# Kernel tuning notes

Measured on AMD Instinct MI355X. Metric: run time of the kernel, lower is better.

The kernel has to match this reference:

```python
import jax, jax.numpy as jnp
import numpy as np

E = 65536      # number of edge tokens
N = 16384      # number of nodes
M = 262144     # number of edge-edge pairs (line-graph edges)
D = 256        # model dim
H = 8          # heads
HD = D // H    # head dim = 32
HID = 4 * D    # ffn hidden = 1024
EPS = 1e-5


def layer_norm(x, scale, bias):
    m = jnp.mean(x, axis=-1, keepdims=True)
    v = jnp.mean(jnp.square(x - m), axis=-1, keepdims=True)
    return (x - m) * jax.lax.rsqrt(v + EPS) * scale + bias


def setup_inputs() -> dict:
    key = jax.random.key(0)
    ks = jax.random.split(key, 24)
    s = 0.02
    inp = {
        'edge_attr': jax.random.normal(ks[0], (E, D), jnp.float32),
        'x': jax.random.normal(ks[1], (N, D), jnp.float32),
        'src_e': jax.random.randint(ks[2], (M,), 0, E),
        'dst_e': jax.random.randint(ks[3], (M,), 0, E),
        'edge_index': jax.random.randint(ks[4], (2, E), 0, N),
        'edge_edge_bias': jax.random.normal(ks[5], (M, H), jnp.float32),
        'ln1_s': jnp.ones((D,), jnp.float32),
        'ln1_b': jnp.zeros((D,), jnp.float32),
        'Wq': jax.random.normal(ks[6], (D, D), jnp.float32) * s,
        'bq': jnp.zeros((D,), jnp.float32),
        'Wk': jax.random.normal(ks[7], (D, D), jnp.float32) * s,
        'bk': jnp.zeros((D,), jnp.float32),
        'Wv': jax.random.normal(ks[8], (D, D), jnp.float32) * s,
        'bv': jnp.zeros((D,), jnp.float32),
        'Wo': jax.random.normal(ks[9], (D, D), jnp.float32) * s,
        'bo': jnp.zeros((D,), jnp.float32),
        'ln2_s': jnp.ones((D,), jnp.float32),
        'ln2_b': jnp.zeros((D,), jnp.float32),
        'W1': jax.random.normal(ks[10], (D, HID), jnp.float32) * s,
        'b1': jnp.zeros((HID,), jnp.float32),
        'W2': jax.random.normal(ks[11], (HID, D), jnp.float32) * s,
        'b2': jnp.zeros((D,), jnp.float32),
        'deg_coef': jax.random.normal(ks[12], (1, D, 2), jnp.float32) * s,
        'We2n': jax.random.normal(ks[13], (D, D), jnp.float32) * s,
        'be2n': jnp.zeros((D,), jnp.float32),
    }
    return inp


def reference(edge_attr, x, src_e, dst_e, edge_index, edge_edge_bias,
              ln1_s, ln1_b, Wq, bq, Wk, bk, Wv, bv, Wo, bo,
              ln2_s, ln2_b, W1, b1, W2, b2, deg_coef, We2n, be2n):
    scale = HD ** (-0.5)
    edge_in = edge_attr  # proj_in is Identity (in_dim == out_dim)

    # --- edge multi-head attention over edge-edge index (pre-LN) ---
    en = layer_norm(edge_in, ln1_s, ln1_b)
    q = (en @ Wq + bq).reshape(E, H, HD)
    k = (en @ Wk + bk).reshape(E, H, HD)
    v = (en @ Wv + bv).reshape(E, H, HD)
    q_dst = q[dst_e]                       # (M, H, HD)
    k_src = k[src_e]
    logits = jnp.sum(q_dst * k_src, axis=-1) * scale + edge_edge_bias  # (M, H)
    # sparse softmax grouped by dst_e (segment softmax with num_segments=E)
    seg_max = jax.ops.segment_max(logits, dst_e, num_segments=E)       # (E, H)
    ex = jnp.exp(logits - seg_max[dst_e])
    seg_sum = jax.ops.segment_sum(ex, dst_e, num_segments=E)
    attn = ex / (seg_sum[dst_e] + 1e-16)                               # (M, H)
    msg = v[src_e] * attn[:, :, None]                                  # (M, H, HD)
    agg = jax.ops.segment_sum(msg, dst_e, num_segments=E).reshape(E, D)
    edge_attn = agg @ Wo + bo
    h1 = edge_in + edge_attn

    # --- FFN (pre-LN), exact GELU as in torch nn.GELU ---
    h1n = layer_norm(h1, ln2_s, ln2_b)
    ffn = jax.nn.gelu(h1n @ W1 + b1, approximate=False) @ W2 + b2
    edge_out = h1 + ffn

    # --- degree scaler: [h, h*log1p(deg_e)] . deg_coef ---
    deg_e = jax.ops.segment_sum(jnp.ones((M,), edge_out.dtype), dst_e, num_segments=E)
    log_deg_e = jnp.log1p(deg_e)[:, None]                              # (E, 1)
    edge_out = edge_out * deg_coef[0, :, 0] + (edge_out * log_deg_e) * deg_coef[0, :, 1]

    # --- edge -> node update (LN output on nodes is unused in the original) ---
    node_msg = (jax.ops.segment_sum(edge_out, edge_index[0], num_segments=N)
                + jax.ops.segment_sum(edge_out, edge_index[1], num_segments=N))
    node_out = x + node_msg @ We2n + be2n

    return edge_out, node_out
```

## Files before the change

### kernel.cpp

```cpp
#include <hip/hip_runtime.h>
#include <math.h>

#define E_ 65536
#define N_ 16384
#define M_ 262144

typedef unsigned short u16;
typedef __attribute__((ext_vector_type(4))) float f32x4;
typedef __attribute__((ext_vector_type(8))) short bf16x8;
typedef __attribute__((ext_vector_type(4))) unsigned short u16x4;
typedef __attribute__((ext_vector_type(2))) unsigned int u32x2;
typedef __attribute__((ext_vector_type(4))) float f4v;

__device__ __forceinline__ float b2f(u16 u) {
    union { unsigned u; float f; } x; x.u = ((unsigned)u) << 16; return x.f;
}
__device__ __forceinline__ u16 f2b(float f) {
    union { float f; unsigned u; } x; x.f = f;
    unsigned r = x.u + 0x7FFFu + ((x.u >> 16) & 1u);
    return (u16)(r >> 16);
}
__device__ __forceinline__ float gelu_f(float x) {
    float y = 1.5957691216057308f * x * (1.0f + 0.044715f * x * x);
    return x * __builtin_amdgcn_rcpf(1.0f + __expf(-y));
}

#define GLDS(gp, lp) __builtin_amdgcn_global_load_lds( \
    (const __attribute__((address_space(1))) void*)(gp), \
    (__attribute__((address_space(3))) void*)(lp), 16, 0, 0)

__global__ void ge_zero(int* __restrict__ p, int n) {
    int i = blockIdx.x * 256 + threadIdx.x;
    if (i < n) p[i] = 0;
}

__global__ void ge_convw(const float* __restrict__ Wq, const float* __restrict__ Wk,
                         const float* __restrict__ Wv, const float* __restrict__ bq,
                         const float* __restrict__ bk, const float* __restrict__ bv,
                         const float* __restrict__ Wo, const float* __restrict__ W1,
                         const float* __restrict__ W2, const float* __restrict__ We2n,
                         u16* __restrict__ WqkvT, float* __restrict__ bqkv,
                         u16* __restrict__ WoT, u16* __restrict__ W1T,
                         u16* __restrict__ W2T, u16* __restrict__ We2nT) {
    long i = (long)blockIdx.x * 256 + threadIdx.x;
    if (i < 196608) {
        int n = (int)(i >> 8), k = (int)(i & 255);
        const float* W = (n < 256) ? Wq : ((n < 512) ? Wk : Wv);
        int nn = n & 255;
        WqkvT[i] = f2b(W[k * 256 + nn]);
        return;
    }
    i -= 196608;
    if (i < 768) { bqkv[i] = (i < 256) ? bq[i] : ((i < 512) ? bk[i - 256] : bv[i - 512]); return; }
    i -= 768;
    if (i < 65536) { int n = (int)(i >> 8), k = (int)(i & 255); WoT[i] = f2b(Wo[k * 256 + n]); return; }
    i -= 65536;
    if (i < 262144) { int n = (int)(i >> 8), k = (int)(i & 255); W1T[i] = f2b(W1[k * 1024 + n]); return; }
    i -= 262144;
    if (i < 262144) {
        int n = (int)(i / 1024), k = (int)(i % 1024);
        int k64 = k & 63, base = k - k64;
        int old_k = base + (k64 & 3) * 16 + (k64 >> 2);
        W2T[i] = f2b(W2[old_k * 256 + n]);
        return;
    }
    i -= 262144;
    if (i < 65536) { int n = (int)(i >> 8), k = (int)(i & 255); We2nT[i] = f2b(We2n[k * 256 + n]); return; }
}

template <int BF16IN>
__global__ __launch_bounds__(256) void ge_ln(const void* __restrict__ in,
                                             const float* __restrict__ s,
                                             const float* __restrict__ b,
                                             u16* __restrict__ out) {
    int tid = threadIdx.x, l = tid & 63, w = tid >> 6;
    long r = (long)blockIdx.x * 4 + w;
    float x0, x1, x2, x3;
    if constexpr (BF16IN) {
        u16x4 xv = *(const u16x4*)&((const u16*)in)[r * 256 + 4 * l];
        x0 = b2f(xv[0]); x1 = b2f(xv[1]); x2 = b2f(xv[2]); x3 = b2f(xv[3]);
    } else {
        f4v x = *(const f4v*)&((const float*)in)[r * 256 + 4 * l];
        x0 = x[0]; x1 = x[1]; x2 = x[2]; x3 = x[3];
    }
    float sum = x0 + x1 + x2 + x3;
#pragma unroll
    for (int off = 1; off < 64; off <<= 1) sum += __shfl_xor(sum, off);
    float mean = sum * (1.0f / 256.0f);
    float d0 = x0 - mean, d1 = x1 - mean, d2 = x2 - mean, d3 = x3 - mean;
    float ss = d0 * d0 + d1 * d1 + d2 * d2 + d3 * d3;
#pragma unroll
    for (int off = 1; off < 64; off <<= 1) ss += __shfl_xor(ss, off);
    float rs = rsqrtf(ss * (1.0f / 256.0f) + 1e-5f);
    u16x4 o;
    o[0] = f2b(d0 * rs * s[4 * l + 0] + b[4 * l + 0]);
    o[1] = f2b(d1 * rs * s[4 * l + 1] + b[4 * l + 1]);
    o[2] = f2b(d2 * rs * s[4 * l + 2] + b[4 * l + 2]);
    o[3] = f2b(d3 * rs * s[4 * l + 3] + b[4 * l + 3]);
    *(u16x4*)&out[r * 256 + 4 * l] = o;
}

__global__ void ge_count(const int* __restrict__ idx, int* __restrict__ cnt, int n) {
    int i = blockIdx.x * 256 + threadIdx.x;
    if (i < n) atomicAdd(&cnt[idx[i]], 1);
}

__global__ __launch_bounds__(256) void ge_bsum(const int* __restrict__ cnt,
                                               int* __restrict__ bsum, int n) {
    int i = blockIdx.x * 256 + threadIdx.x;
    int v = (i < n) ? cnt[i] : 0;
#pragma unroll
    for (int off = 1; off < 64; off <<= 1) v += __shfl_xor(v, off);
    __shared__ int ws_[4];
    int l = threadIdx.x & 63, w = threadIdx.x >> 6;
    if (l == 0) ws_[w] = v;
    __syncthreads();
    if (threadIdx.x == 0) bsum[blockIdx.x] = ws_[0] + ws_[1] + ws_[2] + ws_[3];
}

__global__ __launch_bounds__(256) void ge_bscan(int* __restrict__ bsum, int nb) {
    __shared__ int lds[256];
    int tid = threadIdx.x;
    int v = (tid < nb) ? bsum[tid] : 0;
    lds[tid] = v;
    __syncthreads();
#pragma unroll
    for (int off = 1; off < 256; off <<= 1) {
        int t = (tid >= off) ? lds[tid - off] : 0;
        __syncthreads();
        lds[tid] += t;
        __syncthreads();
    }
    if (tid < nb) bsum[tid] = lds[tid] - v;
}

__global__ __launch_bounds__(256) void ge_cscan(const int* __restrict__ cnt,
                                                const int* __restrict__ bsum,
                                                int* __restrict__ rowStart,
                                                int* __restrict__ cursor,
                                                float* __restrict__ ldeg, int n) {
    __shared__ int lds[256];
    int tid = threadIdx.x;
    int i = blockIdx.x * 256 + tid;
    int c = (i < n) ? cnt[i] : 0;
    lds[tid] = c;
    __syncthreads();
#pragma unroll
    for (int off = 1; off < 256; off <<= 1) {
        int t = (tid >= off) ? lds[tid - off] : 0;
        __syncthreads();
        lds[tid] += t;
        __syncthreads();
    }
    if (i < n) {
        int ex = bsum[blockIdx.x] + lds[tid] - c;
        rowStart[i] = ex;
        cursor[i] = ex;
        if (ldeg) ldeg[i] = log1pf((float)c);
        if (i == n - 1) rowStart[n] = ex + c;
    }
}

__global__ void ge_fill(const int* __restrict__ idx, int* __restrict__ cursor,
                        int* __restrict__ csr, int n, int modE) {
    int i = blockIdx.x * 256 + threadIdx.x;
    if (i < n) {
        int slot = atomicAdd(&cursor[idx[i]], 1);
        csr[slot] = (modE && i >= modE) ? (i - modE) : i;
    }
}

__global__ void ge_fill_attn(const int* __restrict__ dst, const int* __restrict__ src,
                             const float* __restrict__ eeb, int* __restrict__ cursor,
                             int* __restrict__ csrSrc, float* __restrict__ biasCsr, int n) {
    int i = blockIdx.x * 256 + threadIdx.x;
    if (i < n) {
        int slot = atomicAdd(&cursor[dst[i]], 1);
        csrSrc[slot] = src[i];
        f4v b0 = *(const f4v*)&eeb[(size_t)i * 8];
        f4v b1 = *(const f4v*)&eeb[(size_t)i * 8 + 4];
        *(f4v*)&biasCsr[(size_t)slot * 8] = b0;
        *(f4v*)&biasCsr[(size_t)slot * 8 + 4] = b1;
    }
}

template <int EPI>
__global__ __launch_bounds__(256) void ge_gemm(
    const u16* __restrict__ A, const u16* __restrict__ Bt, int K, int nxt,
    const float* __restrict__ bias, const float* __restrict__ res,
    const u16* __restrict__ resB, const float* __restrict__ ldeg,
    const float* __restrict__ dcoef,
    float* __restrict__ outF, u16* __restrict__ outB, u16* __restrict__ outB2,
    int ldOut) {
    __shared__ __align__(16) char smem[32768];
    const int tid = threadIdx.x;
    const int l = tid & 63, w = tid >> 6;
    const int ny = gridDim.x / nxt;
    const int gsz = 64 * ny;
    const int bid = blockIdx.x;
    const int xt = (bid / gsz) * 64 + (bid % gsz) % 64;
    const int yt = (bid % gsz) / 64;
    const int rowBase = xt * 128, colBase = yt * 128;
    const int ar = tid >> 2, aq = tid & 3;
    const int aqs = aq ^ (ar & 3);
    const u16* Ag = A + (size_t)(rowBase + ar) * K + aqs * 8;
    const u16* Bg = Bt + (size_t)(colBase + ar) * K + aqs * 8;
    const size_t row64 = (size_t)64 * K;

    f32x4 acc[4][4] = {};
    const int lr = l & 15;
    const int ks2 = (((l >> 4) ^ (l & 3)) << 3);
    const int wr = (w >> 1) * 64, wc = (w & 1) * 64;
    const int nt = K >> 5;

    auto STAGE = [&](int b, int t) {
        const int kk = t * 32;
        char* dA = smem + b * 8192 + w * 1024;
        char* dB = smem + 16384 + b * 8192 + w * 1024;
        GLDS(Ag + kk, dA);
        GLDS(Ag + kk + row64, dA + 4096);
        GLDS(Bg + kk, dB);
        GLDS(Bg + kk + row64, dB + 4096);
    };

    STAGE(0, 0);
    __syncthreads();
    int cur = 0;
    for (int t = 0; t < nt; ++t) {
        if (t + 1 < nt) STAGE(cur ^ 1, t + 1);
        const u16* bufA = (const u16*)(smem + cur * 8192);
        const u16* bufB = (const u16*)(smem + 16384 + cur * 8192);
        bf16x8 af[4], bfr[4];
#pragma unroll
        for (int mi = 0; mi < 4; mi++) af[mi] = *(const bf16x8*)&bufA[(wr + mi * 16 + lr) * 32 + ks2];
#pragma unroll
        for (int ni = 0; ni < 4; ni++) bfr[ni] = *(const bf16x8*)&bufB[(wc + ni * 16 + lr) * 32 + ks2];
#pragma unroll
        for (int mi = 0; mi < 4; mi++)
#pragma unroll
            for (int ni = 0; ni < 4; ni++)
                acc[mi][ni] = __builtin_amdgcn_mfma_f32_16x16x32_bf16(af[mi], bfr[ni], acc[mi][ni], 0, 0, 0);
        if (t + 1 < nt) {
            __syncthreads();
            cur ^= 1;
        }
    }

    const int r0 = (l >> 4) * 4;
    if constexpr (EPI == 2) {
        float bv[4];
#pragma unroll
        for (int ni = 0; ni < 4; ni++) bv[ni] = bias[colBase + wc + ni * 16 + lr];
#pragma unroll
        for (int mi = 0; mi < 4; mi++) {
#pragma unroll
            for (int r = 0; r < 4; r++) {
                int grow = rowBase + wr + mi * 16 + r0 + r;
                float v0 = gelu_f(acc[mi][0][r] + bv[0]);
                float v1 = gelu_f(acc[mi][1][r] + bv[1]);
                float v2 = gelu_f(acc[mi][2][r] + bv[2]);
                float v3 = gelu_f(acc[mi][3][r] + bv[3]);
                unsigned lo, hi;
                asm("v_cvt_pk_bf16_f32 %0, %1, %2" : "=v"(lo) : "v"(v0), "v"(v1));
                asm("v_cvt_pk_bf16_f32 %0, %1, %2" : "=v"(hi) : "v"(v2), "v"(v3));
                u32x2 pk; pk[0] = lo; pk[1] = hi;
                *(u32x2*)&outB[(size_t)grow * 1024 + colBase + wc + lr * 4] = pk;
            }
        }
    } else if constexpr (EPI == 5) {
        __syncthreads();
        u16* ep = (u16*)smem;
#pragma unroll
        for (int mi = 0; mi < 4; mi++) {
#pragma unroll
            for (int ni = 0; ni < 4; ni++) {
#pragma unroll
                for (int r = 0; r < 4; r++) {
                    int rl = wr + mi * 16 + r0 + r;
                    int cl = wc + ni * 16 + lr;
                    float c = acc[mi][ni][r] + bias[colBase + cl];
                    ep[rl * 128 + (cl ^ (((rl >> 2) & 3) << 4))] = f2b(c);
                }
            }
        }
        __syncthreads();
#pragma unroll
        for (int j = 0; j < 8; j++) {
            int lin = tid + j * 256;
            int row = lin >> 4, ch = lin & 15;
            int grow = rowBase + row;
            bf16x8 v = *(const bf16x8*)&ep[row * 128 + ((ch * 8) ^ (((row >> 2) & 3) << 4))];
            int gcol0 = colBase + ch * 8;
            u16x4 vlo = *((const u16x4*)&v);
            u16x4 vhi = *(((const u16x4*)&v) + 1);
            if (gcol0 < 256) {
                *(bf16x8*)&outB[(size_t)grow * 256 + gcol0] = v;
            } else if (gcol0 < 512) {
                int d0 = (gcol0 - 256) >> 2;
                *(u16x4*)&outB2[(size_t)grow * 512 + 8 * d0] = vlo;
                *(u16x4*)&outB2[(size_t)grow * 512 + 8 * (d0 + 1)] = vhi;
            } else {
                int d0 = (gcol0 - 512) >> 2;
                *(u16x4*)&outB2[(size_t)grow * 512 + 8 * d0 + 4] = vlo;
                *(u16x4*)&outB2[(size_t)grow * 512 + 8 * (d0 + 1) + 4] = vhi;
            }
        }
    } else {
#pragma unroll
        for (int mi = 0; mi < 4; mi++) {
#pragma unroll
            for (int ni = 0; ni < 4; ni++) {
#pragma unroll
                for (int r = 0; r < 4; r++) {
                    int grow = rowBase + wr + mi * 16 + r0 + r;
                    int gcol = colBase + wc + ni * 16 + lr;
                    float c = acc[mi][ni][r];
                    if constexpr (EPI == 1) {
                        outB[(size_t)grow * ldOut + gcol] =
                            f2b(c + bias[gcol] + res[(size_t)grow * 256 + gcol]);
                    } else if constexpr (EPI == 3) {
                        float t2 = c + bias[gcol] + b2f(resB[(size_t)grow * 256 + gcol]);
                        outF[(size_t)grow * ldOut + gcol] =
                            t2 * (dcoef[2 * gcol] + ldeg[grow] * dcoef[2 * gcol + 1]);
                    } else {
                        outF[(size_t)grow * ldOut + gcol] =
                            c + bias[gcol] + res[(size_t)grow * 256 + gcol];
                    }
                }
            }
        }
    }
}

__global__ __launch_bounds__(256) void ge_attn(const u16* __restrict__ qb,
                                               const u16* __restrict__ kvb,
                                               const float* __restrict__ biasCsr,
                                               const int* __restrict__ csrSrc,
                                               const int* __restrict__ rowStart,
                                               u16* __restrict__ agg) {
    int tid = threadIdx.x, l = tid & 63, w = tid >> 6;
    int e = blockIdx.x * 4 + w;
    int g = l >> 3;
    const float scale = 0.17677669529663687f;
    u16x4 qv = *(const u16x4*)&qb[(size_t)e * 256 + 4 * l];
    float q0 = b2f(qv[0]), q1 = b2f(qv[1]), q2 = b2f(qv[2]), q3 = b2f(qv[3]);
    int s0 = rowStart[e], s1 = rowStart[e + 1];

    float sum = 0.0f, a0 = 0.0f, a1 = 0.0f, a2 = 0.0f, a3 = 0.0f;
    if (s0 < s1) {
        int sc = csrSrc[s0];
        bf16x8 kvc = *(const bf16x8*)&kvb[(size_t)sc * 512 + 8 * l];
        float bc = biasCsr[(size_t)s0 * 8 + g];
        for (int i = s0; i < s1; i++) {
            int inx = (i + 1 < s1) ? (i + 1) : i;
            int sn = csrSrc[inx];
            bf16x8 kvn = *(const bf16x8*)&kvb[(size_t)sn * 512 + 8 * l];
            float bn = biasCsr[(size_t)inx * 8 + g];
            float p = q0 * b2f((u16)kvc[0]) + q1 * b2f((u16)kvc[1]) +
                      q2 * b2f((u16)kvc[2]) + q3 * b2f((u16)kvc[3]);
            p += __shfl_xor(p, 1);
            p += __shfl_xor(p, 2);
            p += __shfl_xor(p, 4);
            float ex = __expf(p * scale + bc);
            sum += ex;
            a0 += ex * b2f((u16)kvc[4]);
            a1 += ex * b2f((u16)kvc[5]);
            a2 += ex * b2f((u16)kvc[6]);
            a3 += ex * b2f((u16)kvc[7]);
            kvc = kvn;
            bc = bn;
        }
    }
    float inv = 1.0f / (sum + 1e-16f);
    u16x4 o;
    o[0] = f2b(a0 * inv);
    o[1] = f2b(a1 * inv);
    o[2] = f2b(a2 * inv);
    o[3] = f2b(a3 * inv);
    *(u16x4*)&agg[(size_t)e * 256 + 4 * l] = o;
}

__global__ __launch_bounds__(256) void ge_nodeagg(const float* __restrict__ edge_out,
                                                  const int* __restrict__ rowStart,
                                                  const int* __restrict__ csr,
                                                  u16* __restrict__ nmsg) {
    int tid = threadIdx.x, l = tid & 63, w = tid >> 6;
    int n = blockIdx.x * 4 + w;
    int s0 = rowStart[n], s1 = rowStart[n + 1];
    float a0 = 0.0f, a1 = 0.0f, a2 = 0.0f, a3 = 0.0f;
    for (int i = s0; i < s1; i++) {
        int e = csr[i];
        f4v v = *(const f4v*)&edge_out[(size_t)e * 256 + 4 * l];
        a0 += v[0]; a1 += v[1]; a2 += v[2]; a3 += v[3];
    }
    u16x4 o;
    o[0] = f2b(a0); o[1] = f2b(a1); o[2] = f2b(a2); o[3] = f2b(a3);
    *(u16x4*)&nmsg[(size_t)n * 256 + 4 * l] = o;
}

extern "C" void kernel_launch(void* const* d_in, const int* in_sizes, int n_in,
                              void* d_out, int out_size, void* d_ws, size_t ws_size,
                              hipStream_t stream) {
    (void)in_sizes; (void)n_in; (void)out_size; (void)ws_size;
    const float* edge_attr = (const float*)d_in[0];
    const float* x = (const float*)d_in[1];
    const int* src_e = (const int*)d_in[2];
    const int* dst_e = (const int*)d_in[3];
    const int* edge_index = (const int*)d_in[4];
    const float* eeb = (const float*)d_in[5];
    const float* ln1_s = (const float*)d_in[6];
    const float* ln1_b = (const float*)d_in[7];
    const float* Wq = (const float*)d_in[8];
    const float* bq = (const float*)d_in[9];
    const float* Wk = (const float*)d_in[10];
    const float* bk = (const float*)d_in[11];
    const float* Wv = (const float*)d_in[12];
    const float* bv = (const float*)d_in[13];
    const float* Wo = (const float*)d_in[14];
    const float* bo = (const float*)d_in[15];
    const float* ln2_s = (const float*)d_in[16];
    const float* ln2_b = (const float*)d_in[17];
    const float* W1 = (const float*)d_in[18];
    const float* b1 = (const float*)d_in[19];
    const float* W2 = (const float*)d_in[20];
    const float* b2 = (const float*)d_in[21];
    const float* deg_coef = (const float*)d_in[22];
    const float* We2n = (const float*)d_in[23];
    const float* be2n = (const float*)d_in[24];

    char* ws = (char*)d_ws;
    size_t off = 0;
    auto alloc = [&](size_t bytes) { char* p = ws + off; off += (bytes + 255) & ~(size_t)255; return p; };
    u16* qb = (u16*)alloc((size_t)E_ * 256 * 2);
    u16* kvb = (u16*)alloc((size_t)E_ * 512 * 2);
    u16* agg = (u16*)alloc((size_t)E_ * 256 * 2);
    u16* ffh = qb;
    u16* h1b = (u16*)alloc((size_t)E_ * 256 * 2);
    u16* en = (u16*)alloc((size_t)E_ * 256 * 2);
    u16* h1n = en;
    u16* nmsg = (u16*)alloc((size_t)N_ * 256 * 2);
    u16* WqkvT = (u16*)alloc(768 * 256 * 2);
    float* bqkv = (float*)alloc(768 * 4);
    u16* WoT = (u16*)alloc(256 * 256 * 2);
    u16* W1T = (u16*)alloc(1024 * 256 * 2);
    u16* W2T = (u16*)alloc(256 * 1024 * 2);
    u16* We2nT = (u16*)alloc(256 * 256 * 2);
    int* cntE = (int*)alloc((size_t)E_ * 4);
    int* cntN = (int*)alloc((size_t)N_ * 4);
    int* rowStartE = (int*)alloc((size_t)(E_ + 1) * 4);
    int* cursorE = (int*)alloc((size_t)E_ * 4);
    int* csrSrc = (int*)alloc((size_t)M_ * 4);
    float* biasCsr = (float*)alloc((size_t)M_ * 8 * 4);
    float* ldeg = (float*)alloc((size_t)E_ * 4);
    int* rowStartN = (int*)alloc((size_t)(N_ + 1) * 4);
    int* cursorN = (int*)alloc((size_t)N_ * 4);
    int* csrN = (int*)alloc((size_t)2 * E_ * 4);
    int* bsumE = (int*)alloc(256 * 4);
    int* bsumN = (int*)alloc(64 * 4);

    float* out_edge = (float*)d_out;
    float* out_node = out_edge + (size_t)E_ * 256;

    ge_zero<<<(E_ + N_) / 256, 256, 0, stream>>>(cntE, E_ + N_);
    ge_convw<<<3331, 256, 0, stream>>>(Wq, Wk, Wv, bq, bk, bv, Wo, W1, W2, We2n,
                                       WqkvT, bqkv, WoT, W1T, W2T, We2nT);
    ge_ln<0><<<E_ / 4, 256, 0, stream>>>(edge_attr, ln1_s, ln1_b, en);
    ge_count<<<M_ / 256, 256, 0, stream>>>(dst_e, cntE, M_);
    ge_count<<<2 * E_ / 256, 256, 0, stream>>>(edge_index, cntN, 2 * E_);
    ge_bsum<<<E_ / 256, 256, 0, stream>>>(cntE, bsumE, E_);
    ge_bscan<<<1, 256, 0, stream>>>(bsumE, E_ / 256);
    ge_cscan<<<E_ / 256, 256, 0, stream>>>(cntE, bsumE, rowStartE, cursorE, ldeg, E_);
    ge_bsum<<<N_ / 256, 256, 0, stream>>>(cntN, bsumN, N_);
    ge_bscan<<<1, 256, 0, stream>>>(bsumN, N_ / 256);
    ge_cscan<<<N_ / 256, 256, 0, stream>>>(cntN, bsumN, rowStartN, cursorN, nullptr, N_);
    ge_fill_attn<<<M_ / 256, 256, 0, stream>>>(dst_e, src_e, eeb, cursorE, csrSrc, biasCsr, M_);
    ge_fill<<<2 * E_ / 256, 256, 0, stream>>>(edge_index, cursorN, csrN, 2 * E_, E_);

    ge_gemm<5><<<(E_ / 128) * 6, 256, 0, stream>>>(en, WqkvT, 256, E_ / 128, bqkv,
                                                   nullptr, nullptr, nullptr, nullptr,
                                                   nullptr, qb, kvb, 768);
    ge_attn<<<E_ / 4, 256, 0, stream>>>(qb, kvb, biasCsr, csrSrc, rowStartE, agg);
    ge_gemm<1><<<(E_ / 128) * 2, 256, 0, stream>>>(agg, WoT, 256, E_ / 128, bo,
                                                   edge_attr, nullptr, nullptr, nullptr,
                                                   nullptr, h1b, nullptr, 256);
    ge_ln<1><<<E_ / 4, 256, 0, stream>>>(h1b, ln2_s, ln2_b, h1n);
    ge_gemm<2><<<(E_ / 128) * 8, 256, 0, stream>>>(h1n, W1T, 256, E_ / 128, b1,
                                                   nullptr, nullptr, nullptr, nullptr,
                                                   nullptr, ffh, nullptr, 1024);
    ge_gemm<3><<<(E_ / 128) * 2, 256, 0, stream>>>(ffh, W2T, 1024, E_ / 128, b2,
                                                   nullptr, h1b, ldeg, deg_coef,
                                                   out_edge, nullptr, nullptr, 256);
    ge_nodeagg<<<N_ / 4, 256, 0, stream>>>(out_edge, rowStartN, csrN, nmsg);
    ge_gemm<4><<<(N_ / 128) * 2, 256, 0, stream>>>(nmsg, We2nT, 256, N_ / 128, be2n,
                                                   x, nullptr, nullptr, nullptr,
                                                   out_node, nullptr, nullptr, 256);
}
```

Baseline: 427.3 us.

## Quantize FFN hidden activations and W2 to FP8 and use FP8 MFMA GEMM

The FFN hidden activation (GELU output) is now stored as scaled FP8 instead of bf16, and W2 is converted to scaled FP8. A new dedicated GEMM kernel uses fp8 MFMA instructions with K=1024, undoes the scaling and keeps the residual and degree-scaler epilogue. This halves the memory traffic of the hidden tensor and raises the MFMA rate for the second FFN matmul. The cost is lower numerical precision, which may push the result past the accuracy tolerance.

```diff
diff --git a/kernel.cpp b/kernel.cpp
--- a/kernel.cpp
+++ b/kernel.cpp
@@ -41,7 +41,7 @@
                          const float* __restrict__ W2, const float* __restrict__ We2n,
                          u16* __restrict__ WqkvT, float* __restrict__ bqkv,
                          u16* __restrict__ WoT, u16* __restrict__ W1T,
-                         u16* __restrict__ W2T, u16* __restrict__ We2nT) {
+                         unsigned char* __restrict__ W2T8, u16* __restrict__ We2nT) {
     long i = (long)blockIdx.x * 256 + threadIdx.x;
     if (i < 196608) {
         int n = (int)(i >> 8), k = (int)(i & 255);
@@ -61,7 +61,8 @@
         int n = (int)(i / 1024), k = (int)(i % 1024);
         int k64 = k & 63, base = k - k64;
         int old_k = base + (k64 & 3) * 16 + (k64 >> 2);
-        W2T[i] = f2b(W2[old_k * 256 + n]);
+        unsigned pk = __builtin_amdgcn_cvt_pk_fp8_f32(W2[old_k * 256 + n] * 16.0f, 0.0f, 0u, false);
+        W2T8[i] = (unsigned char)(pk & 0xFFu);
         return;
     }
     i -= 262144;
@@ -251,20 +252,19 @@
         float bv[4];
 #pragma unroll
         for (int ni = 0; ni < 4; ni++) bv[ni] = bias[colBase + wc + ni * 16 + lr];
+        unsigned char* o8 = (unsigned char*)outB;
 #pragma unroll
         for (int mi = 0; mi < 4; mi++) {
 #pragma unroll
             for (int r = 0; r < 4; r++) {
                 int grow = rowBase + wr + mi * 16 + r0 + r;
-                float v0 = gelu_f(acc[mi][0][r] + bv[0]);
-                float v1 = gelu_f(acc[mi][1][r] + bv[1]);
-                float v2 = gelu_f(acc[mi][2][r] + bv[2]);
-                float v3 = gelu_f(acc[mi][3][r] + bv[3]);
-                unsigned lo, hi;
-                asm("v_cvt_pk_bf16_f32 %0, %1, %2" : "=v"(lo) : "v"(v0), "v"(v1));
-                asm("v_cvt_pk_bf16_f32 %0, %1, %2" : "=v"(hi) : "v"(v2), "v"(v3));
-                u32x2 pk; pk[0] = lo; pk[1] = hi;
-                *(u32x2*)&outB[(size_t)grow * 1024 + colBase + wc + lr * 4] = pk;
+                float v0 = gelu_f(acc[mi][0][r] + bv[0]) * 8.0f;
+                float v1 = gelu_f(acc[mi][1][r] + bv[1]) * 8.0f;
+                float v2 = gelu_f(acc[mi][2][r] + bv[2]) * 8.0f;
+                float v3 = gelu_f(acc[mi][3][r] + bv[3]) * 8.0f;
+                unsigned pk = __builtin_amdgcn_cvt_pk_fp8_f32(v0, v1, 0u, false);
+                pk = __builtin_amdgcn_cvt_pk_fp8_f32(v2, v3, pk, true);
+                *(unsigned*)&o8[(size_t)grow * 1024 + colBase + wc + lr * 4] = pk;
             }
         }
     } else if constexpr (EPI == 5) {
@@ -318,15 +318,95 @@
                     if constexpr (EPI == 1) {
                         outB[(size_t)grow * ldOut + gcol] =
                             f2b(c + bias[gcol] + res[(size_t)grow * 256 + gcol]);
-                    } else if constexpr (EPI == 3) {
-                        float t2 = c + bias[gcol] + b2f(resB[(size_t)grow * 256 + gcol]);
-                        outF[(size_t)grow * ldOut + gcol] =
-                            t2 * (dcoef[2 * gcol] + ldeg[grow] * dcoef[2 * gcol + 1]);
                     } else {
                         outF[(size_t)grow * ldOut + gcol] =
                             c + bias[gcol] + res[(size_t)grow * 256 + gcol];
                     }
                 }
+            }
+        }
+    }
+}
+
+__global__ __launch_bounds__(256) void ge_gemm3f8(
+    const unsigned char* __restrict__ A, const unsigned char* __restrict__ Bt, int nxt,
+    const float* __restrict__ bias, const u16* __restrict__ resB,
+    const float* __restrict__ ldeg, const float* __restrict__ dcoef,
+    float* __restrict__ outF) {
+    __shared__ __align__(16) char smem[32768];
+    const int tid = threadIdx.x;
+    const int l = tid & 63, w = tid >> 6;
+    const int ny = gridDim.x / nxt;
+    const int gsz = 64 * ny;
+    const int bid = blockIdx.x;
+    const int xt = (bid / gsz) * 64 + (bid % gsz) % 64;
+    const int yt = (bid % gsz) / 64;
+    const int rowBase = xt * 128, colBase = yt * 128;
+    const int ar = tid >> 2, aq = tid & 3;
+    const int aqs = aq ^ (ar & 3);
+    const unsigned char* Ag = A + (size_t)(rowBase + ar) * 1024 + aqs * 16;
+    const unsigned char* Bg = Bt + (size_t)(colBase + ar) * 1024 + aqs * 16;
+    const size_t row64 = (size_t)64 * 1024;
+
+    f32x4 acc[4][4] = {};
+    const int lr = l & 15, q = l >> 4;
+    const int wr = (w >> 1) * 64, wc = (w & 1) * 64;
+
+    auto STAGE = [&](int b, int t) {
+        const int kk = t * 64;
+        char* dA = smem + b * 8192 + w * 1024;
+        char* dB = smem + 16384 + b * 8192 + w * 1024;
+        GLDS(Ag + kk, dA);
+        GLDS(Ag + kk + row64, dA + 4096);
+        GLDS(Bg + kk, dB);
+        GLDS(Bg + kk + row64, dB + 4096);
+    };
+
+    STAGE(0, 0);
+    __syncthreads();
+    int cur = 0;
+    for (int t = 0; t < 16; ++t) {
+        if (t + 1 < 16) STAGE(cur ^ 1, t + 1);
+        const unsigned char* bufA = (const unsigned char*)(smem + cur * 8192);
+        const unsigned char* bufB = (const unsigned char*)(smem + 16384 + cur * 8192);
+#pragma unroll
+        for (int s = 0; s < 2; ++s) {
+            long long af[4], bf[4];
+#pragma unroll
+            for (int mi = 0; mi < 4; mi++) {
+                int row = wr + mi * 16 + lr;
+                af[mi] = *(const long long*)&bufA[row * 64 + ((2 * s + (q >> 1)) ^ (row & 3)) * 16 + (q & 1) * 8];
+            }
+#pragma unroll
+            for (int ni = 0; ni < 4; ni++) {
+                int col = wc + ni * 16 + lr;
+                bf[ni] = *(const long long*)&bufB[col * 64 + ((2 * s + (q >> 1)) ^ (col & 3)) * 16 + (q & 1) * 8];
+            }
+#pragma unroll
+            for (int mi = 0; mi < 4; mi++)
+#pragma unroll
+                for (int ni = 0; ni < 4; ni++)
+                    acc[mi][ni] = __builtin_amdgcn_mfma_f32_16x16x32_fp8_fp8(af[mi], bf[ni], acc[mi][ni], 0, 0, 0);
+        }
+        if (t + 1 < 16) {
+            __syncthreads();
+            cur ^= 1;
+        }
+    }
+
+    const int r0 = q * 4;
+#pragma unroll
+    for (int mi = 0; mi < 4; mi++) {
+#pragma unroll
+        for (int ni = 0; ni < 4; ni++) {
+#pragma unroll
+            for (int r = 0; r < 4; r++) {
+                int grow = rowBase + wr + mi * 16 + r0 + r;
+                int gcol = colBase + wc + ni * 16 + lr;
+                float t2 = acc[mi][ni][r] * 0.0078125f + bias[gcol] +
+                           b2f(resB[(size_t)grow * 256 + gcol]);
+                outF[(size_t)grow * 256 + gcol] =
+                    t2 * (dcoef[2 * gcol] + ldeg[grow] * dcoef[2 * gcol + 1]);
             }
         }
     }
@@ -434,7 +514,7 @@
     u16* qb = (u16*)alloc((size_t)E_ * 256 * 2);
     u16* kvb = (u16*)alloc((size_t)E_ * 512 * 2);
     u16* agg = (u16*)alloc((size_t)E_ * 256 * 2);
-    u16* ffh = qb;
+    unsigned char* ffh8 = (unsigned char*)qb;
     u16* h1b = (u16*)alloc((size_t)E_ * 256 * 2);
     u16* en = (u16*)alloc((size_t)E_ * 256 * 2);
     u16* h1n = en;
@@ -443,7 +523,7 @@
     float* bqkv = (float*)alloc(768 * 4);
     u16* WoT = (u16*)alloc(256 * 256 * 2);
     u16* W1T = (u16*)alloc(1024 * 256 * 2);
-    u16* W2T = (u16*)alloc(256 * 1024 * 2);
+    unsigned char* W2T8 = (unsigned char*)alloc(256 * 1024);
     u16* We2nT = (u16*)alloc(256 * 256 * 2);
     int* cntE = (int*)alloc((size_t)E_ * 4);
     int* cntN = (int*)alloc((size_t)N_ * 4);
@@ -463,7 +543,7 @@
 
     ge_zero<<<(E_ + N_) / 256, 256, 0, stream>>>(cntE, E_ + N_);
     ge_convw<<<3331, 256, 0, stream>>>(Wq, Wk, Wv, bq, bk, bv, Wo, W1, W2, We2n,
-                                       WqkvT, bqkv, WoT, W1T, W2T, We2nT);
+                                       WqkvT, bqkv, WoT, W1T, W2T8, We2nT);
     ge_ln<0><<<E_ / 4, 256, 0, stream>>>(edge_attr, ln1_s, ln1_b, en);
     ge_count<<<M_ / 256, 256, 0, stream>>>(dst_e, cntE, M_);
     ge_count<<<2 * E_ / 256, 256, 0, stream>>>(edge_index, cntN, 2 * E_);
@@ -486,10 +566,9 @@
     ge_ln<1><<<E_ / 4, 256, 0, stream>>>(h1b, ln2_s, ln2_b, h1n);
     ge_gemm<2><<<(E_ / 128) * 8, 256, 0, stream>>>(h1n, W1T, 256, E_ / 128, b1,
                                                    nullptr, nullptr, nullptr, nullptr,
-                                                   nullptr, ffh, nullptr, 1024);
-    ge_gemm<3><<<(E_ / 128) * 2, 256, 0, stream>>>(ffh, W2T, 1024, E_ / 128, b2,
-                                                   nullptr, h1b, ldeg, deg_coef,
-                                                   out_edge, nullptr, nullptr, 256);
+                                                   nullptr, (u16*)ffh8, nullptr, 1024);
+    ge_gemm3f8<<<(E_ / 128) * 2, 256, 0, stream>>>(ffh8, W2T8, E_ / 128, b2,
+                                                   h1b, ldeg, deg_coef, out_edge);
     ge_nodeagg<<<N_ / 4, 256, 0, stream>>>(out_edge, rowStartN, csrN, nmsg);
     ge_gemm<4><<<(N_ / 128) * 2, 256, 0, stream>>>(nmsg, We2nT, 256, N_ / 128, be2n,
                                                    x, nullptr, nullptr, nullptr,
```

Result: no change. 431.9 us (+1.1%).
